# Performance work log

Measured on AMD Instinct MI355X. Metric: run time of the kernel, lower is better.

The kernel has to match this reference:

```python
import jax, jax.numpy as jnp
import numpy as np

B, N, H = 4, 4096, 64
T1 = 3072  # num_types = [0, 3072, 1024]


def _xavier(key, shape):
    fan_in, fan_out = shape[1], shape[0]
    lim = float(np.sqrt(6.0 / (fan_in + fan_out)))
    return jax.random.uniform(key, shape, jnp.float32, -lim, lim)


def setup_inputs() -> dict:
    key = jax.random.key(0)
    ks = jax.random.split(key, 16)
    adjacency = (jax.random.uniform(ks[0], (N, N)) < 0.05).astype(jnp.float32)
    adjacency = jnp.maximum(adjacency, jnp.eye(N, dtype=jnp.float32))  # avoid all-zero rows
    return {
        "hidden_states": jax.random.normal(ks[1], (B, N, H), jnp.float32),
        "input_states": jax.random.normal(ks[2], (B, 1, 1), jnp.float32),
        "adjacency": adjacency,
        "Wq": _xavier(ks[3], (H, H)),
        "Wk": _xavier(ks[4], (H, H)),
        "Wv": _xavier(ks[5], (H, H)),
        "Wu_inter": _xavier(ks[6], (H, H)),
        "bu_inter": jnp.zeros((H,), jnp.float32),
        "Wt_inter": _xavier(ks[7], (H, H)),
        "bt_inter": jnp.zeros((H,), jnp.float32),
        "Wu_out": _xavier(ks[8], (H, H)),
        "bu_out": jnp.zeros((H,), jnp.float32),
        "Wt_out": _xavier(ks[9], (H, H)),
        "bt_out": jnp.zeros((H,), jnp.float32),
        "step_size": jnp.float32(0.01),
    }


def reference(hidden_states, input_states, adjacency, Wq, Wk, Wv,
              Wu_inter, bu_inter, Wt_inter, bt_inter,
              Wu_out, bu_out, Wt_out, bt_out, step_size):
    # AccumulatorFunction: adjacency-masked QK^T, L2-norm rows (NOT softmax), aggregate V
    mask = adjacency.T  # [N, N]
    q = hidden_states @ Wq.T  # [B, N, H]
    k = hidden_states @ Wk.T
    v = hidden_states @ Wv.T
    rel = jnp.einsum('bnd,bmd->bnm', q, k) * mask  # [B, N, N]
    rel = rel / jnp.linalg.norm(rel, axis=2, keepdims=True)
    acc = jnp.einsum('bnm,bmd->bnd', rel, v)  # [B, N, H]

    # update_hidden_states with num_types = [0, T1, N - T1]
    def branch(h, a, Wu, bu, Wt, bt):
        dt = 2.0 * jax.nn.sigmoid(h @ Wt.T + bt) - 1.0
        return h + step_size * dt * (a @ Wu.T + bu)

    upd_inter = branch(hidden_states[:, :T1], acc[:, :T1],
                       Wu_inter, bu_inter, Wt_inter, bt_inter)
    upd_out = branch(hidden_states[:, T1:], acc[:, T1:],
                     Wu_out, bu_out, Wt_out, bt_out)
    return jnp.concatenate([upd_inter, upd_out], axis=1)  # [B, N, H]
```

## Files before the change

### kernel.cpp

```cpp
#include <hip/hip_runtime.h>
#include <hip/hip_bf16.h>
#include <math.h>

#define Bb 4
#define Nn 4096
#define Hh 64
#define T1c 3072
#define MC 8

typedef unsigned short ushort_t;
typedef __bf16 bf16x8 __attribute__((ext_vector_type(8)));
typedef float floatx4 __attribute__((ext_vector_type(4)));
typedef float floatx16 __attribute__((ext_vector_type(16)));

__device__ ushort_t g_qw[(size_t)Bb * Nn * Hh];
__device__ ushort_t g_kp[(size_t)Bb * Nn * Hh];
__device__ ushort_t g_vp[(size_t)Bb * Nn * Hh];
__device__ ushort_t g_dt[(size_t)Bb * Nn * Hh];
__device__ unsigned long long g_bm[(size_t)Nn * (Nn / 64)];
__device__ float    g_pac[(size_t)Bb * 64 * MC * 64 * 64];
__device__ float    g_pss[(size_t)Bb * 64 * MC * 64];

__device__ __forceinline__ float bf2f(unsigned short u) {
    union { unsigned int i; float f; } c;
    c.i = ((unsigned int)u) << 16;
    return c.f;
}
__device__ __forceinline__ unsigned short f2bf(float f) {
    union { float f; unsigned int i; } c;
    c.f = f;
    unsigned int x = c.i;
    unsigned int r = (x + 0x7fffu + ((x >> 16) & 1u)) >> 16;
    return (unsigned short)r;
}

__device__ __forceinline__ bf16x8 ld8(const void* p, size_t eidx, bool f32) {
    if (f32) {
        const float* fp = (const float*)p + eidx;
        float4 x0 = *(const float4*)fp;
        float4 x1 = *(const float4*)(fp + 4);
        bf16x8 r;
        r[0] = (__bf16)x0.x; r[1] = (__bf16)x0.y; r[2] = (__bf16)x0.z; r[3] = (__bf16)x0.w;
        r[4] = (__bf16)x1.x; r[5] = (__bf16)x1.y; r[6] = (__bf16)x1.z; r[7] = (__bf16)x1.w;
        return r;
    }
    return *(const bf16x8*)((const ushort_t*)p + eidx);
}
__device__ __forceinline__ float ldS(const void* p, size_t eidx, bool f32) {
    return f32 ? ((const float*)p)[eidx] : bf2f(((const ushort_t*)p)[eidx]);
}
__device__ __forceinline__ void stOut(void* p, size_t eidx, float v, bool f32) {
    if (f32) ((float*)p)[eidx] = v;
    else ((ushort_t*)p)[eidx] = f2bf(v);
}

__device__ __forceinline__ floatx4 mfma16(bf16x8 a, bf16x8 b, floatx4 c) {
    return __builtin_amdgcn_mfma_f32_16x16x32_bf16(a, b, c, 0, 0, 0);
}
__device__ __forceinline__ floatx16 mfma32(bf16x8 a, bf16x8 b, floatx16 c) {
    return __builtin_amdgcn_mfma_f32_32x32x16_bf16(a, b, c, 0, 0, 0);
}

__device__ __forceinline__ float fast_tanh(float x) {
    float e = __expf(-2.0f * fabsf(x));
    float t = (1.0f - e) / (1.0f + e);
    return copysignf(t, x);
}

__global__ __launch_bounds__(256) void qkvt_kernel(
    const void* __restrict__ hid, const void* __restrict__ adj,
    const void* __restrict__ Wq, const void* __restrict__ Wk,
    const void* __restrict__ Wv,
    const void* __restrict__ Wti, const void* __restrict__ bti,
    const void* __restrict__ Wto, const void* __restrict__ bto)
{
    const bool F32 = (*(const unsigned*)adj) == 0x3F800000u;

    __shared__ __align__(16) ushort_t stage[2][1024];

    const int bi = blockIdx.x;
    const int b = bi >> 8;
    const int n16 = (bi & 255) << 4;
    const int t = threadIdx.x;
    const int wv = t >> 6, lane = t & 63, l16 = lane & 15, quad = lane >> 4;
    const bool inter = (n16 < T1c);

    const void* W = (wv == 0) ? Wq : (wv == 1) ? Wk : (wv == 2) ? Wv
                    : (inter ? Wti : Wto);
    const void* bt = inter ? bti : bto;

    const size_t hbase = ((size_t)(b * Nn + n16 + l16)) * Hh + quad * 8;
    bf16x8 a0 = ld8(hid, hbase, F32);
    bf16x8 a1 = ld8(hid, hbase + 32, F32);
    floatx4 z = {0.f, 0.f, 0.f, 0.f};

    floatx4 c[4];
#pragma unroll
    for (int ti = 0; ti < 4; ++ti) {
        const size_t wrow = (size_t)(ti * 16 + l16) * 64 + quad * 8;
        bf16x8 w0 = ld8(W, wrow, F32);
        bf16x8 w1 = ld8(W, wrow + 32, F32);
        c[ti] = mfma16(a1, w1, mfma16(a0, w0, z));
    }

    if (wv == 0) {
#pragma unroll
        for (int ti = 0; ti < 4; ++ti)
#pragma unroll
            for (int r = 0; r < 4; ++r)
                g_qw[((size_t)(b * Nn + n16 + quad * 4 + r)) * 64 + ti * 16 + l16] = f2bf(c[ti][r]);
    } else if (wv == 1) {
        ushort_t* st = stage[0];
#pragma unroll
        for (int ti = 0; ti < 4; ++ti)
#pragma unroll
            for (int r = 0; r < 4; ++r)
                st[((ti * 2 + (l16 >> 3)) * 16 + quad * 4 + r) * 8 + (l16 & 7)] = f2bf(c[ti][r]);
        const int mlo0 = n16 & 16;
        const size_t gbase = (size_t)(b * 128 + (n16 >> 5)) * 2048;
#pragma unroll
        for (int piece = 0; piece < 2; ++piece) {
            const int off = lane * 8 + piece * 512;
            const int i = off >> 8;
            const int hh = (off >> 7) & 1;
            const int mj = off & 127;
            *(uint4*)&g_kp[gbase + (size_t)i * 512 + hh * 256 + mlo0 * 8 + mj] =
                *(const uint4*)&st[off];
        }
    } else if (wv == 2) {
        ushort_t* st = stage[1];
#pragma unroll
        for (int ti = 0; ti < 4; ++ti)
#pragma unroll
            for (int r = 0; r < 4; ++r)
                st[(((ti >> 1) * 2 + (quad & 1)) * 32 + (ti & 1) * 16 + l16) * 8
                   + r + 4 * (quad >> 1)] = f2bf(c[ti][r]);
        const size_t gbase = (size_t)(b * 256 + (n16 >> 4)) * 1024;
#pragma unroll
        for (int piece = 0; piece < 2; ++piece) {
            const int off = lane * 8 + piece * 512;
            *(uint4*)&g_vp[gbase + off] = *(const uint4*)&st[off];
        }
    } else {
#pragma unroll
        for (int ti = 0; ti < 4; ++ti) {
            const float btv = ldS(bt, ti * 16 + l16, F32);
#pragma unroll
            for (int r = 0; r < 4; ++r)
                g_dt[((size_t)(b * Nn + n16 + quad * 4 + r)) * 64 + ti * 16 + l16] =
                    f2bf(fast_tanh(0.5f * (c[ti][r] + btv)));
        }
    }
}

__global__ __launch_bounds__(256) void bm_kernel(const void* __restrict__ adj)
{
    const bool F32 = (*(const unsigned*)adj) == 0x3F800000u;
    const int bi = blockIdx.x;
    const int mt = bi & 63;
    const int nc = bi >> 6;
    const int n = nc * 256 + threadIdx.x;
    const int m0 = mt * 64;

    unsigned long long bits = 0ull;
#pragma unroll 8
    for (int j = 0; j < 64; ++j) {
        const float v = ldS(adj, (size_t)(m0 + j) * Nn + n, F32);
        bits |= (unsigned long long)(v != 0.f) << j;
    }
    g_bm[(size_t)n * 64 + mt] = bits;
}

__global__ __launch_bounds__(256, 4) void attn_part_kernel()
{
    const unsigned* bm32 = (const unsigned*)g_bm;

    const int bi = blockIdx.x;
    const int b  = bi >> 8;
    const int mc = (bi >> 5) & 7;
    const int jq = bi & 31;
    const int wv = threadIdx.x >> 6, lane = threadIdx.x & 63;
    const int l32 = lane & 31, h = lane >> 5;
    const int j = jq * 4 + wv;
    const int n0w = j * 32;

    bf16x8 qf[4];
#pragma unroll
    for (int i = 0; i < 4; ++i)
        qf[i] = *(const bf16x8*)&g_qw[((size_t)(b * Nn + n0w + l32)) * 64 + h * 8 + 16 * i];

    floatx16 acc[2];
#pragma unroll
    for (int dt = 0; dt < 2; ++dt)
#pragma unroll
        for (int r = 0; r < 16; ++r) acc[dt][r] = 0.f;
    float ssql = 0.f;

    for (int it = 0; it < 16; ++it) {
        const int mb32 = mc * 16 + it;

        floatx16 s;
#pragma unroll
        for (int r = 0; r < 16; ++r) s[r] = 0.f;
#pragma unroll
        for (int i = 0; i < 4; ++i) {
            bf16x8 kf = *(const bf16x8*)&g_kp[
                ((((size_t)(b * 128 + mb32) * 4 + i) * 2 + h) * 32 + l32) * 8];
            s = mfma32(kf, qf[i], s);
        }

        const unsigned mw = bm32[(size_t)(n0w + l32) * 128 + mb32];
        bf16x8 af0, af1;
#pragma unroll
        for (int r = 0; r < 16; ++r) {
            const int rp = (r & 3) + 8 * (r >> 2) + 4 * h;
            const float sm = ((mw >> rp) & 1u) ? s[r] : 0.f;
            ssql += sm * sm;
            if (r < 8) af0[r] = (__bf16)sm; else af1[r - 8] = (__bf16)sm;
        }

#pragma unroll
        for (int mb = 0; mb < 2; ++mb) {
            const size_t vb = (((size_t)(b * 256 + mb32 * 2 + mb) * 2) * 2 + h) * 32 * 8;
            bf16x8 vf0 = *(const bf16x8*)&g_vp[vb + (size_t)l32 * 8];
            bf16x8 vf1 = *(const bf16x8*)&g_vp[vb + (2 * 32 * 8) + (size_t)l32 * 8];
            if (mb == 0) {
                acc[0] = mfma32(af0, vf0, acc[0]);
                acc[1] = mfma32(af0, vf1, acc[1]);
            } else {
                acc[0] = mfma32(af1, vf0, acc[0]);
                acc[1] = mfma32(af1, vf1, acc[1]);
            }
        }
    }

    ssql += __shfl_xor(ssql, 32, 64);

    const int nt = n0w >> 6;
    const int nl0 = (j & 1) * 32;
    const size_t pbase = ((size_t)(b * 64 + nt) * MC + mc);
#pragma unroll
    for (int dt = 0; dt < 2; ++dt)
#pragma unroll
        for (int r = 0; r < 16; ++r) {
            const int rp = (r & 3) + 8 * (r >> 2) + 4 * h;
            g_pac[(pbase * 64 + nl0 + rp) * 64 + dt * 32 + l32] = acc[dt][r];
        }
    if (h == 0) g_pss[pbase * 64 + nl0 + l32] = ssql;
}

__global__ __launch_bounds__(256) void finish_kernel(
    const void* __restrict__ hid, const void* __restrict__ adj,
    const void* __restrict__ Wui, const void* __restrict__ bui,
    const void* __restrict__ Wuo, const void* __restrict__ buo,
    const void* __restrict__ stepp, void* __restrict__ outp)
{
    const bool F32 = (*(const unsigned*)adj) == 0x3F800000u;

    const int bi = blockIdx.x;
    const int b = bi >> 8;
    const int r16 = bi & 255;
    const int n16 = r16 << 4;
    const int nt = r16 >> 2;
    const int nloc0 = (r16 & 3) << 4;
    const int t = threadIdx.x;
    const int wv = t >> 6, lane = t & 63, l16 = lane & 15, quad = lane >> 4;

    float sv = g_pss[((size_t)(b * 64 + nt) * MC + quad) * 64 + nloc0 + l16]
             + g_pss[((size_t)(b * 64 + nt) * MC + quad + 4) * 64 + nloc0 + l16];
    sv += __shfl_xor(sv, 16, 64);
    sv += __shfl_xor(sv, 32, 64);
    const float inv = (sv > 0.f) ? __frsqrt_rn(sv) : 0.f;

    float s0[8], s1[8];
#pragma unroll
    for (int jj = 0; jj < 8; ++jj) { s0[jj] = 0.f; s1[jj] = 0.f; }
#pragma unroll
    for (int mcq = 0; mcq < MC; ++mcq) {
        const size_t abase =
            (((size_t)(b * 64 + nt) * MC + mcq) * 64 + nloc0 + l16) * 64 + quad * 8;
        float4 x0 = *(const float4*)&g_pac[abase];
        float4 x1 = *(const float4*)&g_pac[abase + 4];
        float4 y0 = *(const float4*)&g_pac[abase + 32];
        float4 y1 = *(const float4*)&g_pac[abase + 36];
        s0[0] += x0.x; s0[1] += x0.y; s0[2] += x0.z; s0[3] += x0.w;
        s0[4] += x1.x; s0[5] += x1.y; s0[6] += x1.z; s0[7] += x1.w;
        s1[0] += y0.x; s1[1] += y0.y; s1[2] += y0.z; s1[3] += y0.w;
        s1[4] += y1.x; s1[5] += y1.y; s1[6] += y1.z; s1[7] += y1.w;
    }
    bf16x8 ua0, ua1;
#pragma unroll
    for (int jj = 0; jj < 8; ++jj) {
        ua0[jj] = (__bf16)(s0[jj] * inv);
        ua1[jj] = (__bf16)(s1[jj] * inv);
    }

    const bool inter = (n16 < T1c);
    const void* Wu = inter ? Wui : Wuo;
    const void* bu = inter ? bui : buo;
    const float step = ldS(stepp, 0, F32);

    const int ti = wv;
    floatx4 z = {0.f, 0.f, 0.f, 0.f};
    const size_t wrow = (size_t)(ti * 16 + l16) * 64 + quad * 8;
    bf16x8 w0 = ld8(Wu, wrow, F32);
    bf16x8 w1 = ld8(Wu, wrow + 32, F32);
    floatx4 u = mfma16(ua1, w1, mfma16(ua0, w0, z));
    const float buv = ldS(bu, ti * 16 + l16, F32);
#pragma unroll
    for (int r = 0; r < 4; ++r) {
        const size_t idx = ((size_t)(b * Nn + n16 + quad * 4 + r)) * 64 + ti * 16 + l16;
        const float hv = ldS(hid, idx, F32);
        const float dtv = bf2f(g_dt[idx]);
        stOut(outp, idx, hv + step * dtv * (u[r] + buv), F32);
    }
}

extern "C" void kernel_launch(void* const* d_in, const int* in_sizes, int n_in,
                              void* d_out, int out_size, void* d_ws, size_t ws_size,
                              hipStream_t stream)
{
    const void* hid = d_in[0];
    const void* adj = d_in[2];
    const void* Wq  = d_in[3];
    const void* Wk  = d_in[4];
    const void* Wv  = d_in[5];
    const void* Wui = d_in[6];
    const void* bui = d_in[7];
    const void* Wti = d_in[8];
    const void* bti = d_in[9];
    const void* Wuo = d_in[10];
    const void* buo = d_in[11];
    const void* Wto = d_in[12];
    const void* bto = d_in[13];
    const void* stepp = d_in[14];

    qkvt_kernel<<<dim3(Bb * (Nn / 16)), dim3(256), 0, stream>>>(
        hid, adj, Wq, Wk, Wv, Wti, bti, Wto, bto);
    bm_kernel<<<dim3(1024), dim3(256), 0, stream>>>(adj);
    attn_part_kernel<<<dim3(1024), dim3(256), 0, stream>>>();
    finish_kernel<<<dim3(Bb * (Nn / 16)), dim3(256), 0, stream>>>(
        hid, adj, Wui, bui, Wuo, buo, stepp, d_out);
}
```

Measured before the change: 193.2 us.

## Merge bitmask build into prep kernel, transpose mask layout, store partials in bf16

Folds the adjacency-bitmask kernel into the QKV/dt projection kernel as extra blocks, which removes one launch and lets the two independent jobs run concurrently. The bitmask is stored as 32-bit words in [mblock][n] order, so lanes in attention read consecutive addresses and loads coalesce. The per-chunk partial accumulators are written and read as bf16 instead of fp32, halving that intermediate traffic at the cost of extra rounding error in the partial sums.

```diff
diff --git a/kernel.cpp b/kernel.cpp
--- a/kernel.cpp
+++ b/kernel.cpp
@@ -17,8 +17,8 @@
 __device__ ushort_t g_kp[(size_t)Bb * Nn * Hh];
 __device__ ushort_t g_vp[(size_t)Bb * Nn * Hh];
 __device__ ushort_t g_dt[(size_t)Bb * Nn * Hh];
-__device__ unsigned long long g_bm[(size_t)Nn * (Nn / 64)];
-__device__ float    g_pac[(size_t)Bb * 64 * MC * 64 * 64];
+__device__ unsigned g_bm32[(size_t)(Nn / 32) * Nn];
+__device__ ushort_t g_pacH[(size_t)Bb * 64 * MC * 64 * 64];
 __device__ float    g_pss[(size_t)Bb * 64 * MC * 64];
 
 __device__ __forceinline__ float bf2f(unsigned short u) {
@@ -67,7 +67,7 @@
     return copysignf(t, x);
 }
 
-__global__ __launch_bounds__(256) void qkvt_kernel(
+__global__ __launch_bounds__(256) void prep_kernel(
     const void* __restrict__ hid, const void* __restrict__ adj,
     const void* __restrict__ Wq, const void* __restrict__ Wk,
     const void* __restrict__ Wv,
@@ -78,6 +78,24 @@
 
     __shared__ __align__(16) ushort_t stage[2][1024];
 
+    if (blockIdx.x >= 1024) {
+        const int bi = blockIdx.x - 1024;
+        const int mt = bi & 63;
+        const int nc = bi >> 6;
+        const int n = nc * 256 + threadIdx.x;
+        const int m0 = mt * 64;
+
+        unsigned long long bits = 0ull;
+#pragma unroll 8
+        for (int j = 0; j < 64; ++j) {
+            const float v = ldS(adj, (size_t)(m0 + j) * Nn + n, F32);
+            bits |= (unsigned long long)(v != 0.f) << j;
+        }
+        g_bm32[(size_t)(2 * mt) * Nn + n] = (unsigned)(bits & 0xffffffffull);
+        g_bm32[(size_t)(2 * mt + 1) * Nn + n] = (unsigned)(bits >> 32);
+        return;
+    }
+
     const int bi = blockIdx.x;
     const int b = bi >> 8;
     const int n16 = (bi & 255) << 4;
@@ -153,28 +171,8 @@
     }
 }
 
-__global__ __launch_bounds__(256) void bm_kernel(const void* __restrict__ adj)
-{
-    const bool F32 = (*(const unsigned*)adj) == 0x3F800000u;
-    const int bi = blockIdx.x;
-    const int mt = bi & 63;
-    const int nc = bi >> 6;
-    const int n = nc * 256 + threadIdx.x;
-    const int m0 = mt * 64;
-
-    unsigned long long bits = 0ull;
-#pragma unroll 8
-    for (int j = 0; j < 64; ++j) {
-        const float v = ldS(adj, (size_t)(m0 + j) * Nn + n, F32);
-        bits |= (unsigned long long)(v != 0.f) << j;
-    }
-    g_bm[(size_t)n * 64 + mt] = bits;
-}
-
 __global__ __launch_bounds__(256, 4) void attn_part_kernel()
 {
-    const unsigned* bm32 = (const unsigned*)g_bm;
-
     const int bi = blockIdx.x;
     const int b  = bi >> 8;
     const int mc = (bi >> 5) & 7;
@@ -209,7 +207,7 @@
             s = mfma32(kf, qf[i], s);
         }
 
-        const unsigned mw = bm32[(size_t)(n0w + l32) * 128 + mb32];
+        const unsigned mw = g_bm32[(size_t)mb32 * Nn + n0w + l32];
         bf16x8 af0, af1;
 #pragma unroll
         for (int r = 0; r < 16; ++r) {
@@ -244,7 +242,7 @@
 #pragma unroll
         for (int r = 0; r < 16; ++r) {
             const int rp = (r & 3) + 8 * (r >> 2) + 4 * h;
-            g_pac[(pbase * 64 + nl0 + rp) * 64 + dt * 32 + l32] = acc[dt][r];
+            g_pacH[(pbase * 64 + nl0 + rp) * 64 + dt * 32 + l32] = f2bf(acc[dt][r]);
         }
     if (h == 0) g_pss[pbase * 64 + nl0 + l32] = ssql;
 }
@@ -279,14 +277,13 @@
     for (int mcq = 0; mcq < MC; ++mcq) {
         const size_t abase =
             (((size_t)(b * 64 + nt) * MC + mcq) * 64 + nloc0 + l16) * 64 + quad * 8;
-        float4 x0 = *(const float4*)&g_pac[abase];
-        float4 x1 = *(const float4*)&g_pac[abase + 4];
-        float4 y0 = *(const float4*)&g_pac[abase + 32];
-        float4 y1 = *(const float4*)&g_pac[abase + 36];
-        s0[0] += x0.x; s0[1] += x0.y; s0[2] += x0.z; s0[3] += x0.w;
-        s0[4] += x1.x; s0[5] += x1.y; s0[6] += x1.z; s0[7] += x1.w;
-        s1[0] += y0.x; s1[1] += y0.y; s1[2] += y0.z; s1[3] += y0.w;
-        s1[4] += y1.x; s1[5] += y1.y; s1[6] += y1.z; s1[7] += y1.w;
+        bf16x8 x = *(const bf16x8*)&g_pacH[abase];
+        bf16x8 y = *(const bf16x8*)&g_pacH[abase + 32];
+#pragma unroll
+        for (int jj = 0; jj < 8; ++jj) {
+            s0[jj] += (float)x[jj];
+            s1[jj] += (float)y[jj];
+        }
     }
     bf16x8 ua0, ua1;
 #pragma unroll
@@ -335,9 +332,8 @@
     const void* bto = d_in[13];
     const void* stepp = d_in[14];
 
-    qkvt_kernel<<<dim3(Bb * (Nn / 16)), dim3(256), 0, stream>>>(
+    prep_kernel<<<dim3(2048), dim3(256), 0, stream>>>(
         hid, adj, Wq, Wk, Wv, Wti, bti, Wto, bto);
-    bm_kernel<<<dim3(1024), dim3(256), 0, stream>>>(adj);
     attn_part_kernel<<<dim3(1024), dim3(256), 0, stream>>>();
     finish_kernel<<<dim3(Bb * (Nn / 16)), dim3(256), 0, stream>>>(
         hid, adj, Wui, bui, Wuo, buo, stepp, d_out);
```

After: 169.1 us (median of 3 runs). 12.5% less time.
